# Performance work log

Measured on AMD Instinct MI355X. Metric: run time of the kernel, lower is better.

The kernel has to match this reference:

```python
import jax, jax.numpy as jnp
import numpy as np

N_WIN = 7
NUM_HEADS = 8
DIM = 256
QK = 256
TOPK = 4
MLP_HID = 4 * DIM
SCALE = QK ** -0.5  # used for both region routing and pixel attention (qk_scale=None)


def _layernorm(x, g, b, eps=1e-6):
    mu = jnp.mean(x, axis=-1, keepdims=True)
    var = jnp.mean(jnp.square(x - mu), axis=-1, keepdims=True)
    return (x - mu) * jax.lax.rsqrt(var + eps) * g + b


def _dwconv(x, w, b):
    # x: NHWC, w: (5,5,1,C) depthwise kernel (torch Conv2d groups=C, padding=2)
    y = jax.lax.conv_general_dilated(
        x, w, window_strides=(1, 1), padding='SAME',
        feature_group_count=x.shape[-1],
        dimension_numbers=('NHWC', 'HWIO', 'NHWC'))
    return y + b


def _bra(x, qkv_w, qkv_b, lepe_w, lepe_b, wo_w, wo_b):
    # BiLevelRoutingAttention, NHWC in/out
    N, H, W, C = x.shape
    j = i = N_WIN
    h, w = H // j, W // i
    p2, w2, m = j * i, h * w, NUM_HEADS
    dq, dv = QK // m, C // m
    # window partition: (N, p2, h, w, C)
    xw = x.reshape(N, j, h, i, w, C).transpose(0, 1, 3, 2, 4, 5).reshape(N, p2, h, w, C)
    qkv = xw @ qkv_w + qkv_b
    q = qkv[..., :QK]            # (N,p2,h,w,QK)
    kv = qkv[..., QK:]           # (N,p2,h,w,QK+C)
    q_pix = q.reshape(N, p2, w2, QK)
    kv_pix = kv.reshape(N, p2, w2, QK + C)
    q_win = jnp.mean(q, axis=(2, 3))                    # (N,p2,QK)
    k_win = jnp.mean(kv[..., :QK], axis=(2, 3))         # (N,p2,QK)
    # LePE: depthwise conv on V in full-image layout
    v_img = kv[..., QK:].reshape(N, j, i, h, w, C).transpose(0, 1, 3, 2, 4, 5).reshape(N, H, W, C)
    lepe = _dwconv(v_img, lepe_w, lepe_b)
    # region-to-region routing, top-k window selection
    logit = jnp.einsum('npc,nqc->npq', q_win * SCALE, k_win)    # (N,p2,p2)
    _, r_idx = jax.lax.top_k(logit, TOPK)                       # (N,p2,TOPK)
    # gather KV of selected windows: (N,p2,TOPK,w2,QK+C)
    kv_sel = kv_pix[jnp.arange(N)[:, None, None], r_idx]
    k_sel = kv_sel[..., :QK].reshape(N, p2, TOPK * w2, m, dq).transpose(0, 1, 3, 2, 4)  # (N,p2,m,kw2,dq)
    v_sel = kv_sel[..., QK:].reshape(N, p2, TOPK * w2, m, dv).transpose(0, 1, 3, 2, 4)  # (N,p2,m,kw2,dv)
    q_h = q_pix.reshape(N, p2, w2, m, dq).transpose(0, 1, 3, 2, 4)                      # (N,p2,m,w2,dq)
    aw = jnp.einsum('npmqd,npmkd->npmqk', q_h * SCALE, k_sel)
    aw = jax.nn.softmax(aw, axis=-1)
    out = jnp.einsum('npmqk,npmkd->npmqd', aw, v_sel)           # (N,p2,m,w2,dv)
    out = out.transpose(0, 1, 3, 2, 4).reshape(N, j, i, h, w, C)
    out = out.transpose(0, 1, 3, 2, 4, 5).reshape(N, H, W, C)
    out = out + lepe
    return out @ wo_w + wo_b


def setup_inputs() -> dict:
    key = jax.random.key(0)
    ks = jax.random.split(key, 8)
    s = 0.02
    return {
        'x': jax.random.normal(ks[0], (8, 56, 56, DIM), dtype=jnp.float32),
        'ln1_g': jnp.ones((DIM,), jnp.float32),
        'ln1_b': jnp.zeros((DIM,), jnp.float32),
        'qkv_w': jax.random.normal(ks[1], (DIM, 2 * QK + DIM), jnp.float32) * s,
        'qkv_b': jnp.zeros((2 * QK + DIM,), jnp.float32),
        'lepe_w': jax.random.normal(ks[2], (5, 5, 1, DIM), jnp.float32) * s,
        'lepe_b': jnp.zeros((DIM,), jnp.float32),
        'wo_w': jax.random.normal(ks[3], (DIM, DIM), jnp.float32) * s,
        'wo_b': jnp.zeros((DIM,), jnp.float32),
        'ln2_g': jnp.ones((DIM,), jnp.float32),
        'ln2_b': jnp.zeros((DIM,), jnp.float32),
        'mlp_w1': jax.random.normal(ks[4], (DIM, MLP_HID), jnp.float32) * s,
        'mlp_b1': jnp.zeros((MLP_HID,), jnp.float32),
        'mlp_w2': jax.random.normal(ks[5], (MLP_HID, DIM), jnp.float32) * s,
        'mlp_b2': jnp.zeros((DIM,), jnp.float32),
    }


def reference(x, ln1_g, ln1_b, qkv_w, qkv_b, lepe_w, lepe_b, wo_w, wo_b,
              ln2_g, ln2_b, mlp_w1, mlp_b1, mlp_w2, mlp_b2):
    x = x + _bra(_layernorm(x, ln1_g, ln1_b), qkv_w, qkv_b, lepe_w, lepe_b, wo_w, wo_b)
    h = _layernorm(x, ln2_g, ln2_b)
    h = jax.nn.gelu(h @ mlp_w1 + mlp_b1, approximate=False) @ mlp_w2 + mlp_b2
    return x + h
```

## Files before the change

kernel.cpp:

```cpp
#include <hip/hip_runtime.h>
#include <hip/hip_bf16.h>

#define NIMG 8
#define HW 56
#define CDIM 256
#define TOK (NIMG*HW*HW)
#define NWIN 49
#define NPW (NIMG*NWIN)
#define ATT_SCALE 0.0625f

typedef __attribute__((ext_vector_type(8))) short short8;
typedef __attribute__((ext_vector_type(4))) short short4v;
typedef __attribute__((ext_vector_type(4))) float f32x4;

static const size_t OFF_WQKV  = 0;
static const size_t OFF_WWO   = 393216;
static const size_t OFF_W1    = 524288;
static const size_t OFF_W2    = 1048576;
static const size_t OFF_XLN   = 1572864;
static const size_t OFF_QKV   = 14417920;
static const size_t OFF_QKWIN = 52953088;
static const size_t OFF_RIDX  = 53755904;
static const size_t OFF_ATTN  = 53762176;
static const size_t OFF_HMID  = OFF_XLN;

__device__ __forceinline__ float gelu_exact(float v) {
    return 0.5f * v * (1.f + erff(v * 0.70710678118654752f));
}
__device__ __forceinline__ short f2bs(float x) {
    __hip_bfloat16 h = __float2bfloat16(x);
    return *(short*)&h;
}
__device__ __forceinline__ float bs2f(short s) {
    return __uint_as_float(((unsigned)(unsigned short)s) << 16);
}
__device__ __forceinline__ void gld16(const short* g, short* l) {
    __builtin_amdgcn_global_load_lds(
        (const __attribute__((address_space(1))) void*)g,
        (__attribute__((address_space(3))) void*)l, 16, 0, 0);
}

__global__ __launch_bounds__(256) void transpose_cast4_k(const float* __restrict__ s0,
                                                         const float* __restrict__ s1,
                                                         const float* __restrict__ s2,
                                                         const float* __restrict__ s3,
                                                         __hip_bfloat16* __restrict__ d0,
                                                         __hip_bfloat16* __restrict__ d1,
                                                         __hip_bfloat16* __restrict__ d2,
                                                         __hip_bfloat16* __restrict__ d3) {
    int b = blockIdx.x;
    const float* src; __hip_bfloat16* dst; int K, N, l;
    if (b < 192)      { src = s0; dst = d0; K = 256;  N = 768;  l = b; }
    else if (b < 256) { src = s1; dst = d1; K = 256;  N = 256;  l = b - 192; }
    else if (b < 512) { src = s2; dst = d2; K = 256;  N = 1024; l = b - 256; }
    else              { src = s3; dst = d3; K = 1024; N = 256;  l = b - 512; }
    int nx = N / 32;
    int n0 = (l % nx) * 32, k0 = (l / nx) * 32;
    __shared__ float t[32][33];
    int tx = threadIdx.x & 31, ty = threadIdx.x >> 5;
    #pragma unroll
    for (int i = 0; i < 32; i += 8)
        t[ty + i][tx] = src[(size_t)(k0 + ty + i) * N + n0 + tx];
    __syncthreads();
    #pragma unroll
    for (int i = 0; i < 32; i += 8)
        dst[(size_t)(n0 + ty + i) * K + k0 + tx] = __float2bfloat16(t[tx][ty + i]);
}

__global__ __launch_bounds__(256) void ln_bf_k(const float* __restrict__ in,
                                               const float* __restrict__ g,
                                               const float* __restrict__ b,
                                               short* __restrict__ out, int remap) {
    int t = blockIdx.x * 4 + (threadIdx.x >> 6);
    int lane = threadIdx.x & 63;
    float4 v = *(const float4*)(in + (size_t)t * 256 + lane * 4);
    float s = v.x + v.y + v.z + v.w;
    float s2 = v.x * v.x + v.y * v.y + v.z * v.z + v.w * v.w;
    #pragma unroll
    for (int o = 32; o > 0; o >>= 1) {
        s  += __shfl_xor(s, o);
        s2 += __shfl_xor(s2, o);
    }
    float mu = s * (1.f / 256.f);
    float rstd = rsqrtf(s2 * (1.f / 256.f) - mu * mu + 1e-6f);
    float4 gv = *(const float4*)(g + lane * 4);
    float4 bv = *(const float4*)(b + lane * 4);
    short4v o;
    o[0] = f2bs((v.x - mu) * rstd * gv.x + bv.x);
    o[1] = f2bs((v.y - mu) * rstd * gv.y + bv.y);
    o[2] = f2bs((v.z - mu) * rstd * gv.z + bv.z);
    o[3] = f2bs((v.w - mu) * rstd * gv.w + bv.w);
    size_t tb;
    if (remap) {
        int n = t / 3136, rem = t % 3136, y = rem / 56, x = rem % 56;
        int p = (y >> 3) * 7 + (x >> 3);
        int si = (y & 7) * 8 + (x & 7);
        tb = (size_t)(n * 49 + p) * 64 + si;
    } else {
        tb = (size_t)t;
    }
    *(short4v*)(out + tb * 256 + lane * 4) = o;
}

template<int MODE>
__global__ __launch_bounds__(256) void gemm64(const short* __restrict__ A,
                                              const short* __restrict__ Bt,
                                              const float* __restrict__ bias,
                                              const float* __restrict__ res,
                                              void* Cv, int M, int N, int K) {
    const int bn = blockIdx.x * 128;
    const int bm = blockIdx.y * 64;
    const int tid = threadIdx.x;
    const int wave = tid >> 6, lane = tid & 63;
    const int l15 = lane & 15, quad = lane >> 4;
    const int wm = (wave & 1) * 32, wn = (wave >> 1) * 64;

    __shared__ __align__(16) short smem[6144];
    short* As = smem;
    short* Bs = smem + 2048;

    f32x4 acc[2][4];
    #pragma unroll
    for (int i = 0; i < 2; ++i)
        #pragma unroll
        for (int j = 0; j < 4; ++j) acc[i][j] = (f32x4){0.f, 0.f, 0.f, 0.f};

    const int crow = lane >> 2;
    const int ckq = (lane & 3) * 8;
    const short* ga  = A  + (size_t)(bm + wave * 16 + crow) * K + ckq;
    const short* gb0 = Bt + (size_t)(bn + wave * 16 + crow) * K + ckq;
    const short* gb1 = gb0 + (size_t)64 * K;
    short* la  = As + wave * 512;
    short* lb0 = Bs + wave * 512;
    short* lb1 = Bs + 2048 + wave * 512;

    for (int k0 = 0; k0 < K; k0 += 32) {
        gld16(ga + k0, la);
        gld16(gb0 + k0, lb0);
        gld16(gb1 + k0, lb1);
        __syncthreads();
        short8 af[2], bfr[4];
        #pragma unroll
        for (int i = 0; i < 2; ++i)
            af[i] = *(const short8*)&As[(wm + i * 16 + l15) * 32 + quad * 8];
        #pragma unroll
        for (int j = 0; j < 4; ++j)
            bfr[j] = *(const short8*)&Bs[(wn + j * 16 + l15) * 32 + quad * 8];
        #pragma unroll
        for (int i = 0; i < 2; ++i)
            #pragma unroll
            for (int j = 0; j < 4; ++j)
                acc[i][j] = __builtin_amdgcn_mfma_f32_16x16x32_bf16(af[i], bfr[j], acc[i][j], 0, 0, 0);
        __syncthreads();
    }

    if (MODE == 1) {
        #pragma unroll
        for (int i = 0; i < 2; ++i) {
            int row = bm + wm + i * 16 + quad * 4;
            #pragma unroll
            for (int j = 0; j < 4; ++j) {
                int col = bn + wn + j * 16 + l15;
                float bia = bias[col];
                #pragma unroll
                for (int r = 0; r < 4; ++r) {
                    size_t idx = (size_t)(row + r) * N + col;
                    ((float*)Cv)[idx] = acc[i][j][r] + bia + res[idx];
                }
            }
        }
    } else {
        float biasv[4];
        #pragma unroll
        for (int j = 0; j < 4; ++j) biasv[j] = bias[bn + wn + j * 16 + l15];
        short* ep = &smem[wave * 1280];
        short* outp = (short*)Cv;
        #pragma unroll
        for (int p = 0; p < 2; ++p) {
            #pragma unroll
            for (int i = 0; i < 2; ++i)
                #pragma unroll
                for (int jj = 0; jj < 2; ++jj) {
                    int j = p * 2 + jj;
                    #pragma unroll
                    for (int r = 0; r < 4; ++r) {
                        float v = acc[i][j][r] + biasv[j];
                        if (MODE == 2) v = gelu_exact(v);
                        ep[(i * 16 + quad * 4 + r) * 40 + jj * 16 + l15] = f2bs(v);
                    }
                }
            __builtin_amdgcn_s_waitcnt(0);
            int c = lane & 3;
            #pragma unroll
            for (int rr = 0; rr < 2; ++rr) {
                int row = rr * 16 + (lane >> 2);
                short8 v = *(const short8*)&ep[row * 40 + c * 8];
                *(short8*)&outp[(size_t)(bm + wm + row) * N + bn + wn + p * 32 + c * 8] = v;
            }
            __builtin_amdgcn_s_waitcnt(0);
        }
    }
}

__global__ __launch_bounds__(256) void win_means_k(const short* __restrict__ qkv,
                                                   float* __restrict__ qkwin) {
    int w = blockIdx.x;
    int cg = (threadIdx.x & 63) * 8;
    int sp = threadIdx.x >> 6;
    float s[8] = {0.f, 0.f, 0.f, 0.f, 0.f, 0.f, 0.f, 0.f};
    const short* base = qkv + (size_t)w * 64 * 768 + cg;
    for (int si = sp; si < 64; si += 4) {
        short8 v = *(const short8*)(base + (size_t)si * 768);
        #pragma unroll
        for (int i = 0; i < 8; ++i) s[i] += bs2f(v[i]);
    }
    __shared__ float red[4][512];
    #pragma unroll
    for (int i = 0; i < 8; ++i) red[sp][cg + i] = s[i];
    __syncthreads();
    for (int c = threadIdx.x; c < 512; c += 256) {
        float t = red[0][c] + red[1][c] + red[2][c] + red[3][c];
        qkwin[(size_t)w * 512 + c] = t * (1.f / 64.f);
    }
}

__global__ __launch_bounds__(64) void route_k(const float* __restrict__ qkwin,
                                              int* __restrict__ ridx) {
    int w = blockIdx.x;
    int n = w / 49;
    int tid = threadIdx.x;
    __shared__ float qv[256];
    __shared__ float lg[49];
    for (int i = tid; i < 256; i += 64) qv[i] = qkwin[(size_t)w * 512 + i] * ATT_SCALE;
    __syncthreads();
    if (tid < 49) {
        const float* kp = qkwin + (size_t)(n * 49 + tid) * 512 + 256;
        float d = 0.f;
        for (int cc = 0; cc < 256; ++cc) d += qv[cc] * kp[cc];
        lg[tid] = d;
    }
    __syncthreads();
    if (tid == 0) {
        #pragma unroll
        for (int t = 0; t < 4; ++t) {
            float best = -1e30f; int bi = 0;
            for (int j = 0; j < 49; ++j)
                if (lg[j] > best) { best = lg[j]; bi = j; }
            lg[bi] = -1e30f;
            ridx[w * 4 + t] = bi;
        }
    }
}

__global__ __launch_bounds__(256) void attn_mfma_k(const short* __restrict__ qkv,
                                                   const int* __restrict__ ridx,
                                                   short* __restrict__ attn) {
    const int blk = blockIdx.x;
    const int w = blk >> 3, h = blk & 7;
    const int n = w / 49;
    const int tid = threadIdx.x;
    const int wave = tid >> 6, lane = tid & 63;
    const int l15 = lane & 15, quad = lane >> 4;

    __shared__ __align__(16) short smem[25344];
    short* Vt = smem;
    short* Ks = smem + 8448;
    short* Ps = smem + 8448;
    __shared__ int rs4[4];
    if (tid < 4) rs4[tid] = ridx[w * 4 + tid];
    __syncthreads();

    {
        int s = tid >> 2, kq = (tid & 3) * 8;
        #pragma unroll
        for (int u = 0; u < 4; ++u) {
            int key = u * 64 + s;
            const short* src = qkv + ((size_t)(n * 49 + rs4[u]) * 64 + s) * 768 + 256 + h * 32 + kq;
            *(short8*)&Ks[key * 40 + kq] = *(const short8*)src;
        }
    }
    {
        int kp = tid & 127, dh = tid >> 7;
        int k0 = kp * 2;
        int t = k0 >> 6, s = k0 & 63;
        const short* src0 = qkv + ((size_t)(n * 49 + rs4[t]) * 64 + s) * 768 + 512 + h * 32 + dh * 16;
        const short* src1 = src0 + 768;
        short8 a0 = *(const short8*)src0, a1 = *(const short8*)(src0 + 8);
        short8 b0 = *(const short8*)src1, b1 = *(const short8*)(src1 + 8);
        #pragma unroll
        for (int d = 0; d < 8; ++d) {
            *(unsigned*)&Vt[(dh * 16 + d) * 264 + k0] =
                (unsigned)(unsigned short)a0[d] | ((unsigned)(unsigned short)b0[d] << 16);
            *(unsigned*)&Vt[(dh * 16 + 8 + d) * 264 + k0] =
                (unsigned)(unsigned short)a1[d] | ((unsigned)(unsigned short)b1[d] << 16);
        }
    }
    __syncthreads();

    const short* qp = qkv + ((size_t)w * 64 + wave * 16 + l15) * 768 + h * 32 + quad * 8;
    short8 qf = *(const short8*)qp;

    f32x4 st[16];
    #pragma unroll
    for (int j = 0; j < 16; ++j) {
        short8 kf = *(const short8*)&Ks[(j * 16 + l15) * 40 + quad * 8];
        st[j] = __builtin_amdgcn_mfma_f32_16x16x32_bf16(kf, qf, (f32x4){0.f, 0.f, 0.f, 0.f}, 0, 0, 0);
    }

    float mx = -1e30f;
    #pragma unroll
    for (int j = 0; j < 16; ++j)
        #pragma unroll
        for (int r = 0; r < 4; ++r) mx = fmaxf(mx, st[j][r]);
    mx = fmaxf(mx, __shfl_xor(mx, 16));
    mx = fmaxf(mx, __shfl_xor(mx, 32));

    __syncthreads();

    short* pw = &Ps[wave * 16 * 264];
    float sum = 0.f;
    #pragma unroll
    for (int j = 0; j < 16; ++j) {
        short4v pv;
        #pragma unroll
        for (int r = 0; r < 4; ++r) {
            float p = __expf((st[j][r] - mx) * ATT_SCALE);
            sum += p;
            pv[r] = f2bs(p);
        }
        *(short4v*)&pw[l15 * 264 + j * 16 + quad * 4] = pv;
    }
    sum += __shfl_xor(sum, 16);
    sum += __shfl_xor(sum, 32);
    float inv = 1.f / sum;
    __builtin_amdgcn_s_waitcnt(0);

    f32x4 oc[2] = {(f32x4){0.f,0.f,0.f,0.f}, (f32x4){0.f,0.f,0.f,0.f}};
    #pragma unroll
    for (int kk = 0; kk < 8; ++kk) {
        short8 pf = *(const short8*)&pw[l15 * 264 + kk * 32 + quad * 8];
        #pragma unroll
        for (int jj = 0; jj < 2; ++jj) {
            short8 vf = *(const short8*)&Vt[(jj * 16 + l15) * 264 + kk * 32 + quad * 8];
            oc[jj] = __builtin_amdgcn_mfma_f32_16x16x32_bf16(vf, pf, oc[jj], 0, 0, 0);
        }
    }

    short* op = attn + ((size_t)w * 64 + wave * 16 + l15) * 256 + h * 32;
    #pragma unroll
    for (int jj = 0; jj < 2; ++jj) {
        short4v o4;
        #pragma unroll
        for (int r = 0; r < 4; ++r) o4[r] = f2bs(oc[jj][r] * inv);
        *(short4v*)&op[jj * 16 + quad * 4] = o4;
    }
}

__global__ __launch_bounds__(256) void lepe_k(const short* __restrict__ qkv,
                                              const short* __restrict__ attn,
                                              const float* __restrict__ lw,
                                              const float* __restrict__ lb,
                                              short* __restrict__ ywo) {
    int t = blockIdx.x * 8 + (threadIdx.x >> 5);
    int c0 = (threadIdx.x & 31) * 8;
    int n = t / 3136, rem = t % 3136, y = rem / 56, x = rem % 56;
    float sum[8];
    {
        float4 b0 = *(const float4*)(lb + c0), b1 = *(const float4*)(lb + c0 + 4);
        sum[0] = b0.x; sum[1] = b0.y; sum[2] = b0.z; sum[3] = b0.w;
        sum[4] = b1.x; sum[5] = b1.y; sum[6] = b1.z; sum[7] = b1.w;
    }
    #pragma unroll
    for (int ky = 0; ky < 5; ++ky) {
        int yy = y + ky - 2;
        if ((unsigned)yy >= 56u) continue;
        #pragma unroll
        for (int kx = 0; kx < 5; ++kx) {
            int xx = x + kx - 2;
            if ((unsigned)xx >= 56u) continue;
            int p = (yy >> 3) * 7 + (xx >> 3);
            int si = (yy & 7) * 8 + (xx & 7);
            short8 v = *(const short8*)(qkv + ((size_t)(n * 49 + p) * 64 + si) * 768 + 512 + c0);
            const float* wp = lw + (ky * 5 + kx) * 256 + c0;
            float4 w0 = *(const float4*)wp, w1 = *(const float4*)(wp + 4);
            sum[0] += bs2f(v[0]) * w0.x; sum[1] += bs2f(v[1]) * w0.y;
            sum[2] += bs2f(v[2]) * w0.z; sum[3] += bs2f(v[3]) * w0.w;
            sum[4] += bs2f(v[4]) * w1.x; sum[5] += bs2f(v[5]) * w1.y;
            sum[6] += bs2f(v[6]) * w1.z; sum[7] += bs2f(v[7]) * w1.w;
        }
    }
    int p0 = (y >> 3) * 7 + (x >> 3);
    int s0 = (y & 7) * 8 + (x & 7);
    short8 a = *(const short8*)(attn + ((size_t)(n * 49 + p0) * 64 + s0) * 256 + c0);
    short8 o;
    #pragma unroll
    for (int i = 0; i < 8; ++i) o[i] = f2bs(sum[i] + bs2f(a[i]));
    *(short8*)(ywo + (size_t)t * 256 + c0) = o;
}

extern "C" void kernel_launch(void* const* d_in, const int* in_sizes, int n_in,
                              void* d_out, int out_size, void* d_ws, size_t ws_size,
                              hipStream_t stream) {
    const float* x      = (const float*)d_in[0];
    const float* ln1_g  = (const float*)d_in[1];
    const float* ln1_b  = (const float*)d_in[2];
    const float* qkv_w  = (const float*)d_in[3];
    const float* qkv_b  = (const float*)d_in[4];
    const float* lepe_w = (const float*)d_in[5];
    const float* lepe_b = (const float*)d_in[6];
    const float* wo_w   = (const float*)d_in[7];
    const float* wo_b   = (const float*)d_in[8];
    const float* ln2_g  = (const float*)d_in[9];
    const float* ln2_b  = (const float*)d_in[10];
    const float* mlp_w1 = (const float*)d_in[11];
    const float* mlp_b1 = (const float*)d_in[12];
    const float* mlp_w2 = (const float*)d_in[13];
    const float* mlp_b2 = (const float*)d_in[14];
    float* out = (float*)d_out;

    char* ws = (char*)d_ws;
    __hip_bfloat16* wqkvT = (__hip_bfloat16*)(ws + OFF_WQKV);
    __hip_bfloat16* wwoT  = (__hip_bfloat16*)(ws + OFF_WWO);
    __hip_bfloat16* w1T   = (__hip_bfloat16*)(ws + OFF_W1);
    __hip_bfloat16* w2T   = (__hip_bfloat16*)(ws + OFF_W2);
    short* xln   = (short*)(ws + OFF_XLN);
    short* qkvb  = (short*)(ws + OFF_QKV);
    float* qkwin = (float*)(ws + OFF_QKWIN);
    int*   ridx  = (int*)(ws + OFF_RIDX);
    short* attnb = (short*)(ws + OFF_ATTN);
    short* ywo   = (short*)(ws + OFF_XLN);
    short* h2    = (short*)(ws + OFF_ATTN);
    short* hmid  = (short*)(ws + OFF_HMID);

    transpose_cast4_k<<<768, 256, 0, stream>>>(qkv_w, wo_w, mlp_w1, mlp_w2,
                                               wqkvT, wwoT, w1T, w2T);
    ln_bf_k<<<TOK/4, 256, 0, stream>>>(x, ln1_g, ln1_b, xln, 1);
    gemm64<0><<<dim3(6, 392), 256, 0, stream>>>(xln, (const short*)wqkvT,
                                                qkv_b, nullptr, qkvb, TOK, 768, 256);
    win_means_k<<<NPW, 256, 0, stream>>>(qkvb, qkwin);
    route_k<<<NPW, 64, 0, stream>>>(qkwin, ridx);
    attn_mfma_k<<<NPW * 8, 256, 0, stream>>>(qkvb, ridx, attnb);
    lepe_k<<<TOK/8, 256, 0, stream>>>(qkvb, attnb, lepe_w, lepe_b, ywo);
    gemm64<1><<<dim3(2, 392), 256, 0, stream>>>(ywo, (const short*)wwoT,
                                                wo_b, x, out, TOK, 256, 256);
    ln_bf_k<<<TOK/4, 256, 0, stream>>>(out, ln2_g, ln2_b, h2, 0);
    gemm64<2><<<dim3(8, 392), 256, 0, stream>>>(h2, (const short*)w1T,
                                                mlp_b1, nullptr, hmid, TOK, 1024, 256);
    gemm64<1><<<dim3(2, 392), 256, 0, stream>>>(hmid, (const short*)w2T,
                                                mlp_b2, out, out, TOK, 256, 1024);
}
```

Measured before the change: 300.5 us.

## Double-buffer LDS tiles in GEMM and XOR-swizzle layout to avoid bank conflicts

The GEMM main loop now uses two LDS buffers, so the global-to-LDS loads for the next K slice are issued before the MFMAs on the current slice run, with one barrier per iteration instead of two. The column chunk within each row is XOR-swizzled on both the load and read sides to reduce LDS bank conflicts. An extra barrier before the epilogue protects the LDS reuse. LDS use doubles, which may lower occupancy.

```diff
diff --git a/kernel.cpp b/kernel.cpp
--- a/kernel.cpp
+++ b/kernel.cpp
@@ -102,6 +102,23 @@
     *(short4v*)(out + tb * 256 + lane * 4) = o;
 }
 
+__device__ __forceinline__ void mfma_step(const short* As, const short* Bs,
+                                          int wm, int wn, int l15, int swr,
+                                          f32x4 acc[2][4]) {
+    short8 af[2], bfr[4];
+    #pragma unroll
+    for (int i = 0; i < 2; ++i)
+        af[i] = *(const short8*)&As[(wm + i * 16 + l15) * 32 + swr];
+    #pragma unroll
+    for (int j = 0; j < 4; ++j)
+        bfr[j] = *(const short8*)&Bs[(wn + j * 16 + l15) * 32 + swr];
+    #pragma unroll
+    for (int i = 0; i < 2; ++i)
+        #pragma unroll
+        for (int j = 0; j < 4; ++j)
+            acc[i][j] = __builtin_amdgcn_mfma_f32_16x16x32_bf16(af[i], bfr[j], acc[i][j], 0, 0, 0);
+}
+
 template<int MODE>
 __global__ __launch_bounds__(256) void gemm64(const short* __restrict__ A,
                                               const short* __restrict__ Bt,
@@ -115,9 +132,7 @@
     const int l15 = lane & 15, quad = lane >> 4;
     const int wm = (wave & 1) * 32, wn = (wave >> 1) * 64;
 
-    __shared__ __align__(16) short smem[6144];
-    short* As = smem;
-    short* Bs = smem + 2048;
+    __shared__ __align__(16) short smem[12288];
 
     f32x4 acc[2][4];
     #pragma unroll
@@ -126,32 +141,35 @@
         for (int j = 0; j < 4; ++j) acc[i][j] = (f32x4){0.f, 0.f, 0.f, 0.f};
 
     const int crow = lane >> 2;
-    const int ckq = (lane & 3) * 8;
+    const int ckq = ((lane & 3) ^ ((lane >> 3) & 3)) * 8;
     const short* ga  = A  + (size_t)(bm + wave * 16 + crow) * K + ckq;
     const short* gb0 = Bt + (size_t)(bn + wave * 16 + crow) * K + ckq;
     const short* gb1 = gb0 + (size_t)64 * K;
-    short* la  = As + wave * 512;
-    short* lb0 = Bs + wave * 512;
-    short* lb1 = Bs + 2048 + wave * 512;
-
-    for (int k0 = 0; k0 < K; k0 += 32) {
-        gld16(ga + k0, la);
-        gld16(gb0 + k0, lb0);
-        gld16(gb1 + k0, lb1);
-        __syncthreads();
-        short8 af[2], bfr[4];
-        #pragma unroll
-        for (int i = 0; i < 2; ++i)
-            af[i] = *(const short8*)&As[(wm + i * 16 + l15) * 32 + quad * 8];
-        #pragma unroll
-        for (int j = 0; j < 4; ++j)
-            bfr[j] = *(const short8*)&Bs[(wn + j * 16 + l15) * 32 + quad * 8];
-        #pragma unroll
-        for (int i = 0; i < 2; ++i)
-            #pragma unroll
-            for (int j = 0; j < 4; ++j)
-                acc[i][j] = __builtin_amdgcn_mfma_f32_16x16x32_bf16(af[i], bfr[j], acc[i][j], 0, 0, 0);
-        __syncthreads();
+    const int swr = (quad ^ ((l15 >> 1) & 3)) * 8;
+
+    gld16(ga,  smem + wave * 512);
+    gld16(gb0, smem + 2048 + wave * 512);
+    gld16(gb1, smem + 4096 + wave * 512);
+    asm volatile("s_waitcnt vmcnt(0)" ::: "memory");
+    __builtin_amdgcn_s_barrier();
+    asm volatile("" ::: "memory");
+
+    int cur = 0;
+    for (int k0 = 32; k0 < K; k0 += 32) {
+        short* nb = smem + (cur ^ 1) * 6144;
+        gld16(ga  + k0, nb + wave * 512);
+        gld16(gb0 + k0, nb + 2048 + wave * 512);
+        gld16(gb1 + k0, nb + 4096 + wave * 512);
+        const short* As = smem + cur * 6144;
+        mfma_step(As, As + 2048, wm, wn, l15, swr, acc);
+        asm volatile("s_waitcnt vmcnt(0) lgkmcnt(0)" ::: "memory");
+        __builtin_amdgcn_s_barrier();
+        asm volatile("" ::: "memory");
+        cur ^= 1;
+    }
+    {
+        const short* As = smem + cur * 6144;
+        mfma_step(As, As + 2048, wm, wn, l15, swr, acc);
     }
 
     if (MODE == 1) {
@@ -170,6 +188,9 @@
             }
         }
     } else {
+        asm volatile("s_waitcnt lgkmcnt(0)" ::: "memory");
+        __builtin_amdgcn_s_barrier();
+        asm volatile("" ::: "memory");
         float biasv[4];
         #pragma unroll
         for (int j = 0; j < 4; ++j) biasv[j] = bias[bn + wn + j * 16 + l15];
```

Result: no change. 299.7 us (-0.3%).
